# Optimization experiments

Measured on AMD Instinct MI355X. Metric: run time of the kernel, lower is better.

The kernel has to match this reference:

```python
import jax, jax.numpy as jnp
import numpy as np
import math

D_MODEL = 2048
ORDER = 64
GAMMA_MIN, GAMMA_MAX = 0.01, 0.1
SEQ_LEN = 2048


def setup_inputs() -> dict:
    key = jax.random.key(0)
    k1, k2 = jax.random.split(key)
    # gamma = log(uniform in [gamma_min, gamma_max))
    gamma = jnp.log(
        jax.random.uniform(k1, (D_MODEL, ORDER), dtype=jnp.float32)
        * (GAMMA_MAX - GAMMA_MIN) + GAMMA_MIN
    )
    R = 0.1 * jax.random.normal(k2, (D_MODEL, ORDER), dtype=jnp.float32) / math.sqrt(ORDER)
    p = -jnp.ones((D_MODEL, ORDER), dtype=jnp.float32)
    return {"gamma": gamma, "R": R, "p": p, "L": SEQ_LEN}


def reference(gamma, R, p, L):
    # t: (1, 1, L) broadcast as (L,) against (d, o, 1)
    t = jnp.arange(L, dtype=jnp.float32)          # (L,)
    logp = -jnp.exp(p)                            # (d, o), strictly negative -> decaying modes
    glogp = logp * jnp.exp(gamma)                 # (d, o)
    h = jnp.exp(glogp[..., None] * t)             # (d, o, L)
    h = jnp.einsum('do,dot->dt', R, h)            # (d, L)
    return h[None]                                # (1, d, L)
```

## Files before the change

kernel.cpp:

```cpp
#include <hip/hip_runtime.h>
#include <hip/hip_bf16.h>


#define DMODEL 2048
#define ORDER  64
#define SEQLEN 2048

typedef __attribute__((ext_vector_type(8))) __bf16 bf16x8;
typedef __attribute__((ext_vector_type(16))) float f32x16;

__global__ __launch_bounds__(256) void imf_mfma_kernel(
    const float* __restrict__ gamma,
    const float* __restrict__ R,
    const float* __restrict__ p,
    float* __restrict__ out)
{
    const int tid  = threadIdx.x;
    const int wave = tid >> 6;
    const int lane = tid & 63;
    const int d    = blockIdx.x * 4 + wave;

    __shared__ float2 cst[4][ORDER];

    {
        const int i = blockIdx.x * 256 + tid;
        const float LOG2E = 1.44269504088896340736f;
        const float gg = gamma[i];
        const float pp = p[i];
        const float rr = R[i];
        const float gl2 = -__builtin_amdgcn_exp2f((pp + gg) * LOG2E) * LOG2E;
        cst[wave][lane] = make_float2(gl2, rr);
    }
    __syncthreads();

    const int   row = lane & 31;
    const int   hl  = lane >> 5;
    const float frow = (float)row;

    f32x16 acc0, acc1;
#pragma unroll
    for (int r = 0; r < 16; ++r) { acc0[r] = 0.0f; acc1[r] = 0.0f; }

#pragma unroll
    for (int kk = 0; kk < 4; ++kk) {
        const int ob = 16 * kk + 8 * hl;
        bf16x8 ah, al, a2h, a2l, bh, bl;
#pragma unroll
        for (int j = 0; j < 8; ++j) {
            const float2 c = cst[wave][ob + j];
            const float gl2 = c.x, rr = c.y;
            const float a  = rr * __builtin_amdgcn_exp2f(gl2 * (32.0f * frow));
            const float a2 = rr * __builtin_amdgcn_exp2f(gl2 * (32.0f * (frow + 32.0f)));
            const float b  = __builtin_amdgcn_exp2f(gl2 * frow);

            const __bf16 ah_j = (__bf16)a;
            const __bf16 a2h_j = (__bf16)a2;
            const __bf16 bh_j = (__bf16)b;
            ah[j]  = ah_j;   al[j]  = (__bf16)(a  - (float)ah_j);
            a2h[j] = a2h_j;  a2l[j] = (__bf16)(a2 - (float)a2h_j);
            bh[j]  = bh_j;   bl[j]  = (__bf16)(b  - (float)bh_j);
        }
        acc0 = __builtin_amdgcn_mfma_f32_32x32x16_bf16(ah,  bh, acc0, 0, 0, 0);
        acc0 = __builtin_amdgcn_mfma_f32_32x32x16_bf16(al,  bh, acc0, 0, 0, 0);
        acc0 = __builtin_amdgcn_mfma_f32_32x32x16_bf16(ah,  bl, acc0, 0, 0, 0);
        acc1 = __builtin_amdgcn_mfma_f32_32x32x16_bf16(a2h, bh, acc1, 0, 0, 0);
        acc1 = __builtin_amdgcn_mfma_f32_32x32x16_bf16(a2l, bh, acc1, 0, 0, 0);
        acc1 = __builtin_amdgcn_mfma_f32_32x32x16_bf16(a2h, bl, acc1, 0, 0, 0);
    }

    float* od = out + (size_t)d * SEQLEN;
#pragma unroll
    for (int r = 0; r < 16; ++r) {
        const int t1 = (r & 3) + 8 * (r >> 2) + 4 * hl;
        od[32 * t1 + row]        = acc0[r];
        od[32 * (t1 + 32) + row] = acc1[r];
    }
}

extern "C" void kernel_launch(void* const* d_in, const int* in_sizes, int n_in,
                              void* d_out, int out_size, void* d_ws, size_t ws_size,
                              hipStream_t stream) {
    const float* gamma = (const float*)d_in[0];
    const float* R     = (const float*)d_in[1];
    const float* p     = (const float*)d_in[2];
    float* out = (float*)d_out;

    imf_mfma_kernel<<<dim3(DMODEL / 4), dim3(256), 0, stream>>>(gamma, R, p, out);
}
```

Measured before the change: 11.88 us.

## Split each channel's sequence across two waves using precomputed shifted residues

After: 12.73 us. 1.07x slower.

```diff
diff --git a/kernel.cpp b/kernel.cpp
--- a/kernel.cpp
+++ b/kernel.cpp
@@ -15,65 +15,63 @@
     const float* __restrict__ p,
     float* __restrict__ out)
 {
-    const int tid  = threadIdx.x;
-    const int wave = tid >> 6;
-    const int lane = tid & 63;
-    const int d    = blockIdx.x * 4 + wave;
+    const int tid   = threadIdx.x;
+    const int wave  = tid >> 6;
+    const int lane  = tid & 63;
+    const int dslot = wave >> 1;
+    const int th    = wave & 1;
+    const int d     = blockIdx.x * 2 + dslot;
 
-    __shared__ float2 cst[4][ORDER];
+    __shared__ float4 cst[2][ORDER];
 
-    {
-        const int i = blockIdx.x * 256 + tid;
+    if (tid < 128) {
+        const int i = blockIdx.x * 128 + tid;
         const float LOG2E = 1.44269504088896340736f;
         const float gg = gamma[i];
         const float pp = p[i];
         const float rr = R[i];
         const float gl2 = -__builtin_amdgcn_exp2f((pp + gg) * LOG2E) * LOG2E;
-        cst[wave][lane] = make_float2(gl2, rr);
+        const float rl  = rr * __builtin_amdgcn_exp2f(gl2 * 1024.0f);
+        cst[tid >> 6][tid & 63] = make_float4(gl2, rr, rl, 0.0f);
     }
     __syncthreads();
 
-    const int   row = lane & 31;
-    const int   hl  = lane >> 5;
+    const int   row  = lane & 31;
+    const int   hl   = lane >> 5;
     const float frow = (float)row;
 
-    f32x16 acc0, acc1;
+    f32x16 acc;
 #pragma unroll
-    for (int r = 0; r < 16; ++r) { acc0[r] = 0.0f; acc1[r] = 0.0f; }
+    for (int r = 0; r < 16; ++r) acc[r] = 0.0f;
 
 #pragma unroll
     for (int kk = 0; kk < 4; ++kk) {
         const int ob = 16 * kk + 8 * hl;
-        bf16x8 ah, al, a2h, a2l, bh, bl;
+        bf16x8 ah, al, bh, bl;
 #pragma unroll
         for (int j = 0; j < 8; ++j) {
-            const float2 c = cst[wave][ob + j];
-            const float gl2 = c.x, rr = c.y;
-            const float a  = rr * __builtin_amdgcn_exp2f(gl2 * (32.0f * frow));
-            const float a2 = rr * __builtin_amdgcn_exp2f(gl2 * (32.0f * (frow + 32.0f)));
-            const float b  = __builtin_amdgcn_exp2f(gl2 * frow);
+            const float4 c = cst[dslot][ob + j];
+            const float u    = c.x * frow;
+            const float b    = __builtin_amdgcn_exp2f(u);
+            const float e32  = __builtin_amdgcn_exp2f(32.0f * u);
+            const float reff = th ? c.z : c.y;
+            const float a    = reff * e32;
 
-            const __bf16 ah_j = (__bf16)a;
-            const __bf16 a2h_j = (__bf16)a2;
-            const __bf16 bh_j = (__bf16)b;
-            ah[j]  = ah_j;   al[j]  = (__bf16)(a  - (float)ah_j);
-            a2h[j] = a2h_j;  a2l[j] = (__bf16)(a2 - (float)a2h_j);
-            bh[j]  = bh_j;   bl[j]  = (__bf16)(b  - (float)bh_j);
+            const __bf16 ahj = (__bf16)a;
+            const __bf16 bhj = (__bf16)b;
+            ah[j] = ahj;  al[j] = (__bf16)(a - (float)ahj);
+            bh[j] = bhj;  bl[j] = (__bf16)(b - (float)bhj);
         }
-        acc0 = __builtin_amdgcn_mfma_f32_32x32x16_bf16(ah,  bh, acc0, 0, 0, 0);
-        acc0 = __builtin_amdgcn_mfma_f32_32x32x16_bf16(al,  bh, acc0, 0, 0, 0);
-        acc0 = __builtin_amdgcn_mfma_f32_32x32x16_bf16(ah,  bl, acc0, 0, 0, 0);
-        acc1 = __builtin_amdgcn_mfma_f32_32x32x16_bf16(a2h, bh, acc1, 0, 0, 0);
-        acc1 = __builtin_amdgcn_mfma_f32_32x32x16_bf16(a2l, bh, acc1, 0, 0, 0);
-        acc1 = __builtin_amdgcn_mfma_f32_32x32x16_bf16(a2h, bl, acc1, 0, 0, 0);
+        acc = __builtin_amdgcn_mfma_f32_32x32x16_bf16(ah, bh, acc, 0, 0, 0);
+        acc = __builtin_amdgcn_mfma_f32_32x32x16_bf16(al, bh, acc, 0, 0, 0);
+        acc = __builtin_amdgcn_mfma_f32_32x32x16_bf16(ah, bl, acc, 0, 0, 0);
     }
 
-    float* od = out + (size_t)d * SEQLEN;
+    float* od = out + (size_t)d * SEQLEN + 1024 * th;
 #pragma unroll
     for (int r = 0; r < 16; ++r) {
         const int t1 = (r & 3) + 8 * (r >> 2) + 4 * hl;
-        od[32 * t1 + row]        = acc0[r];
-        od[32 * (t1 + 32) + row] = acc1[r];
+        od[32 * t1 + row] = acc[r];
     }
 }
 
@@ -85,5 +83,5 @@
     const float* p     = (const float*)d_in[2];
     float* out = (float*)d_out;
 
-    imf_mfma_kernel<<<dim3(DMODEL / 4), dim3(256), 0, stream>>>(gamma, R, p, out);
+    imf_mfma_kernel<<<dim3(DMODEL / 2), dim3(256), 0, stream>>>(gamma, R, p, out);
 }
```
